# Kernel tuning notes

Measured on AMD Instinct MI355X. Metric: run time of the kernel, lower is better.

## Reference

```python
import jax, jax.numpy as jnp
import numpy as np

NBINS = 128


def setup_inputs() -> dict:
    key = jax.random.key(0)
    feats = jax.random.normal(key, (100000, 8), dtype=jnp.float32)
    return {"feats": feats}


def reference(feats):
    # feats: [N, V]. setup=True path: fmin/fmax computed from feats itself.
    nvars = feats.shape[1]
    fmin = feats.min(axis=0)  # [V]
    fmax = feats.max(axis=0)  # [V]
    # torch.linspace(min, max, nbins) per variable -> [V, NBINS]
    t = jnp.arange(NBINS, dtype=feats.dtype) / (NBINS - 1)
    lin = fmin[:, None] + (fmax - fmin)[:, None] * t[None, :]
    step = lin[:, 1] - lin[:, 0]  # [V]
    # dense diff matrix, rounded to 6 decimals (np.around = round-half-even)
    diff = jnp.round((lin[None, :, :] - feats[:, :, None]) * 1e6) / 1e6  # [N, V, NBINS]
    # torch: cur_diff[cur_diff > 0] = cur_diff.min()  (min over that var's whole [N, NBINS] slab)
    mn = diff.min(axis=(0, 2), keepdims=True)  # [1, V, 1]
    masked = jnp.where(diff > 0, mn, diff)
    bins = jnp.argmax(masked, axis=2)  # [N, V], first max like torch
    # value of the chosen bin edge per sample/var
    vals = lin[jnp.arange(nvars)[None, :], bins]  # [N, V]
    regs = jnp.clip(feats - vals, 0.0, None) / step[None, :]
    return bins, regs
```

## Files before the change

### kernel.cpp

```cpp
#include <hip/hip_runtime.h>
#include <math.h>

#define NV 8
#define NBINS 128
#define GRID_A 64
#define GRID_Q 1024
#define BLK_Q 256


__global__ __launch_bounds__(256) void k_colminmax(const float* __restrict__ feats,
                                                   float* __restrict__ ws, int n) {
    const int tid = threadIdx.x;
    const int gt = blockIdx.x * blockDim.x + tid;
    const int nth = blockDim.x * gridDim.x;
    float lmin[NV], lmax[NV];
#pragma unroll
    for (int c = 0; c < NV; ++c) { lmin[c] = __builtin_inff(); lmax[c] = -__builtin_inff(); }
    const int n4 = n >> 2;
    const float4* f4 = (const float4*)feats;
    if (((gt << 2) & 7) == 0) {
        for (int q = gt; q < n4; q += nth) {
            float4 v = f4[q];
            lmin[0] = fminf(lmin[0], v.x); lmax[0] = fmaxf(lmax[0], v.x);
            lmin[1] = fminf(lmin[1], v.y); lmax[1] = fmaxf(lmax[1], v.y);
            lmin[2] = fminf(lmin[2], v.z); lmax[2] = fmaxf(lmax[2], v.z);
            lmin[3] = fminf(lmin[3], v.w); lmax[3] = fmaxf(lmax[3], v.w);
        }
    } else {
        for (int q = gt; q < n4; q += nth) {
            float4 v = f4[q];
            lmin[4] = fminf(lmin[4], v.x); lmax[4] = fmaxf(lmax[4], v.x);
            lmin[5] = fminf(lmin[5], v.y); lmax[5] = fmaxf(lmax[5], v.y);
            lmin[6] = fminf(lmin[6], v.z); lmax[6] = fmaxf(lmax[6], v.z);
            lmin[7] = fminf(lmin[7], v.w); lmax[7] = fmaxf(lmax[7], v.w);
        }
    }
    for (int i = (n4 << 2) + gt; i < n; i += nth) {
        float v = feats[i];
        int c = i & 7;
#pragma unroll
        for (int cc = 0; cc < NV; ++cc)
            if (cc == c) { lmin[cc] = fminf(lmin[cc], v); lmax[cc] = fmaxf(lmax[cc], v); }
    }
#pragma unroll
    for (int c = 0; c < NV; ++c) {
        float mn = lmin[c], mx = lmax[c];
#pragma unroll
        for (int m = 32; m >= 1; m >>= 1) {
            mn = fminf(mn, __shfl_xor(mn, m));
            mx = fmaxf(mx, __shfl_xor(mx, m));
        }
        lmin[c] = mn; lmax[c] = mx;
    }
    __shared__ float smin[4][NV], smax[4][NV];
    const int wave = tid >> 6, lane = tid & 63;
    if (lane == 0) {
#pragma unroll
        for (int c = 0; c < NV; ++c) { smin[wave][c] = lmin[c]; smax[wave][c] = lmax[c]; }
    }
    __syncthreads();
    if (tid < NV) {
        float mn = fminf(fminf(smin[0][tid], smin[1][tid]), fminf(smin[2][tid], smin[3][tid]));
        float mx = fmaxf(fmaxf(smax[0][tid], smax[1][tid]), fmaxf(smax[2][tid], smax[3][tid]));
        ws[blockIdx.x * NV + tid] = mn;
        ws[GRID_A * NV + blockIdx.x * NV + tid] = mx;
    }
}

__global__ __launch_bounds__(BLK_Q) void k_quantize2(const float* __restrict__ feats,
                                                     const float* __restrict__ ws,
                                                     float* __restrict__ out, int n) {
    __shared__ float sgmin[NV], sgmax[NV];
    __shared__ float slin[NV * 129];
    __shared__ float sfmin[NV], sstep[NV], srstep[NV];
    const int tid = threadIdx.x;

    if (tid < 64) {
        const float4* w4 = (const float4*)ws;
        float4 a  = w4[2 * tid];
        float4 b4 = w4[2 * tid + 1];
        float4 c4 = w4[2 * GRID_A + 2 * tid];
        float4 d4 = w4[2 * GRID_A + 2 * tid + 1];
        float mn[NV] = {a.x, a.y, a.z, a.w, b4.x, b4.y, b4.z, b4.w};
        float mx[NV] = {c4.x, c4.y, c4.z, c4.w, d4.x, d4.y, d4.z, d4.w};
#pragma unroll
        for (int c = 0; c < NV; ++c) {
#pragma unroll
            for (int m = 32; m >= 1; m >>= 1) {
                mn[c] = fminf(mn[c], __shfl_xor(mn[c], m));
                mx[c] = fmaxf(mx[c], __shfl_xor(mx[c], m));
            }
        }
        if (tid == 0) {
#pragma unroll
            for (int c = 0; c < NV; ++c) { sgmin[c] = mn[c]; sgmax[c] = mx[c]; }
        }
    }
    __syncthreads();

    for (int e = tid; e < NV * NBINS; e += BLK_Q) {
        int v = e >> 7;
        int b = e & 127;
        float fmn = sgmin[v];
        float range = __fsub_rn(sgmax[v], fmn);
        float tb = __fdiv_rn((float)b, 127.0f);
        slin[v * 129 + b] = __fadd_rn(fmn, __fmul_rn(range, tb));
    }
    __syncthreads();
    if (tid < NV) {
        float s0 = slin[tid * 129 + 0];
        float s1 = slin[tid * 129 + 1];
        sfmin[tid] = s0;
        float st = __fsub_rn(s1, s0);
        sstep[tid] = st;
        srstep[tid] = __fdiv_rn(1.0f, st);
    }
    __syncthreads();

    const int gid = blockIdx.x * BLK_Q + tid;
    const int nth = GRID_Q * BLK_Q;
    const int v = gid & 7;
    const float fmn = sfmin[v];
    const float step = sstep[v];
    const float rstep = srstep[v];
    const float* lv = &slin[v * 129];
    for (int i = gid; i < n; i += nth) {
        const float feat = feats[i];
        int b = (int)floorf(__fmul_rn(__fsub_rn(feat, fmn), rstep));
        b = b < 0 ? 0 : (b > 127 ? 127 : b);
        while (b < NBINS - 1 &&
               rintf(__fmul_rn(__fsub_rn(lv[b + 1], feat), 1.0e6f)) <= 0.0f) ++b;
        while (b > 0 &&
               rintf(__fmul_rn(__fsub_rn(lv[b], feat), 1.0e6f)) > 0.0f) --b;
        const float val = lv[b];
        const float reg = __fdiv_rn(fmaxf(__fsub_rn(feat, val), 0.0f), step);
        out[i] = (float)b;
        out[n + i] = reg;
    }
}

extern "C" void kernel_launch(void* const* d_in, const int* in_sizes, int n_in,
                              void* d_out, int out_size, void* d_ws, size_t ws_size,
                              hipStream_t stream) {
    const float* feats = (const float*)d_in[0];
    float* ws = (float*)d_ws;
    float* out = (float*)d_out;
    const int n = in_sizes[0];
    k_colminmax<<<GRID_A, 256, 0, stream>>>(feats, ws, n);
    k_quantize2<<<GRID_Q, BLK_Q, 0, stream>>>(feats, ws, out, n);
}
```

Before: 67.18 us.

## Vectorize quantize with float4, prefetch inputs before setup, unroll min/max loads

The quantize kernel now handles four features per thread as float4 loads and stores. It issues the first two float4 loads before the shared-memory setup so their latency overlaps the per-block linspace construction. The grid shrinks so that two prefetched chunks cover the input. The column min/max kernel unrolls its strided loop by four to keep more loads in flight. The cost is more register pressure, plus a loop-invariant per-variable lookup that now becomes a per-element shared-memory index.

```diff
diff --git a/kernel.cpp b/kernel.cpp
--- a/kernel.cpp
+++ b/kernel.cpp
@@ -4,7 +4,7 @@
 #define NV 8
 #define NBINS 128
 #define GRID_A 64
-#define GRID_Q 1024
+#define GRID_Q 400
 #define BLK_Q 256
 
 
@@ -18,8 +18,23 @@
     for (int c = 0; c < NV; ++c) { lmin[c] = __builtin_inff(); lmax[c] = -__builtin_inff(); }
     const int n4 = n >> 2;
     const float4* f4 = (const float4*)feats;
+    int q = gt;
     if (((gt << 2) & 7) == 0) {
-        for (int q = gt; q < n4; q += nth) {
+        for (; q + 3 * nth < n4; q += 4 * nth) {
+            float4 a = f4[q];
+            float4 b = f4[q + nth];
+            float4 c = f4[q + 2 * nth];
+            float4 d = f4[q + 3 * nth];
+            lmin[0] = fminf(fminf(lmin[0], fminf(a.x, b.x)), fminf(c.x, d.x));
+            lmax[0] = fmaxf(fmaxf(lmax[0], fmaxf(a.x, b.x)), fmaxf(c.x, d.x));
+            lmin[1] = fminf(fminf(lmin[1], fminf(a.y, b.y)), fminf(c.y, d.y));
+            lmax[1] = fmaxf(fmaxf(lmax[1], fmaxf(a.y, b.y)), fmaxf(c.y, d.y));
+            lmin[2] = fminf(fminf(lmin[2], fminf(a.z, b.z)), fminf(c.z, d.z));
+            lmax[2] = fmaxf(fmaxf(lmax[2], fmaxf(a.z, b.z)), fmaxf(c.z, d.z));
+            lmin[3] = fminf(fminf(lmin[3], fminf(a.w, b.w)), fminf(c.w, d.w));
+            lmax[3] = fmaxf(fmaxf(lmax[3], fmaxf(a.w, b.w)), fmaxf(c.w, d.w));
+        }
+        for (; q < n4; q += nth) {
             float4 v = f4[q];
             lmin[0] = fminf(lmin[0], v.x); lmax[0] = fmaxf(lmax[0], v.x);
             lmin[1] = fminf(lmin[1], v.y); lmax[1] = fmaxf(lmax[1], v.y);
@@ -27,7 +42,21 @@
             lmin[3] = fminf(lmin[3], v.w); lmax[3] = fmaxf(lmax[3], v.w);
         }
     } else {
-        for (int q = gt; q < n4; q += nth) {
+        for (; q + 3 * nth < n4; q += 4 * nth) {
+            float4 a = f4[q];
+            float4 b = f4[q + nth];
+            float4 c = f4[q + 2 * nth];
+            float4 d = f4[q + 3 * nth];
+            lmin[4] = fminf(fminf(lmin[4], fminf(a.x, b.x)), fminf(c.x, d.x));
+            lmax[4] = fmaxf(fmaxf(lmax[4], fmaxf(a.x, b.x)), fmaxf(c.x, d.x));
+            lmin[5] = fminf(fminf(lmin[5], fminf(a.y, b.y)), fminf(c.y, d.y));
+            lmax[5] = fmaxf(fmaxf(lmax[5], fmaxf(a.y, b.y)), fmaxf(c.y, d.y));
+            lmin[6] = fminf(fminf(lmin[6], fminf(a.z, b.z)), fminf(c.z, d.z));
+            lmax[6] = fmaxf(fmaxf(lmax[6], fmaxf(a.z, b.z)), fmaxf(c.z, d.z));
+            lmin[7] = fminf(fminf(lmin[7], fminf(a.w, b.w)), fminf(c.w, d.w));
+            lmax[7] = fmaxf(fmaxf(lmax[7], fmaxf(a.w, b.w)), fmaxf(c.w, d.w));
+        }
+        for (; q < n4; q += nth) {
             float4 v = f4[q];
             lmin[4] = fminf(lmin[4], v.x); lmax[4] = fmaxf(lmax[4], v.x);
             lmin[5] = fminf(lmin[5], v.y); lmax[5] = fmaxf(lmax[5], v.y);
@@ -64,6 +93,42 @@
         float mx = fmaxf(fmaxf(smax[0][tid], smax[1][tid]), fmaxf(smax[2][tid], smax[3][tid]));
         ws[blockIdx.x * NV + tid] = mn;
         ws[GRID_A * NV + blockIdx.x * NV + tid] = mx;
+    }
+}
+
+__device__ __forceinline__ void proc4(float4 fv, int q, const float* __restrict__ slin,
+                                      const float* __restrict__ sfmin,
+                                      const float* __restrict__ sstep,
+                                      const float* __restrict__ srstep,
+                                      float* __restrict__ out, int n) {
+    const int v0 = (q << 2) & 7;
+    const int i0 = q << 2;
+    float fe[4] = {fv.x, fv.y, fv.z, fv.w};
+    float bins[4], regs[4];
+#pragma unroll
+    for (int j = 0; j < 4; ++j) {
+        const int v = v0 + j;
+        const float* lv = &slin[v * 129];
+        const float feat = fe[j];
+        const float fmn = sfmin[v];
+        const float step = sstep[v];
+        const float rstep = srstep[v];
+        int b = (int)floorf(__fmul_rn(__fsub_rn(feat, fmn), rstep));
+        b = b < 0 ? 0 : (b > 127 ? 127 : b);
+        while (b < NBINS - 1 &&
+               rintf(__fmul_rn(__fsub_rn(lv[b + 1], feat), 1.0e6f)) <= 0.0f) ++b;
+        while (b > 0 &&
+               rintf(__fmul_rn(__fsub_rn(lv[b], feat), 1.0e6f)) > 0.0f) --b;
+        const float val = lv[b];
+        bins[j] = (float)b;
+        regs[j] = __fdiv_rn(fmaxf(__fsub_rn(feat, val), 0.0f), step);
+    }
+    *(float4*)(out + i0) = make_float4(bins[0], bins[1], bins[2], bins[3]);
+    if ((n & 3) == 0) {
+        *(float4*)(out + n + i0) = make_float4(regs[0], regs[1], regs[2], regs[3]);
+    } else {
+        out[n + i0 + 0] = regs[0]; out[n + i0 + 1] = regs[1];
+        out[n + i0 + 2] = regs[2]; out[n + i0 + 3] = regs[3];
     }
 }
 
@@ -74,6 +139,16 @@
     __shared__ float slin[NV * 129];
     __shared__ float sfmin[NV], sstep[NV], srstep[NV];
     const int tid = threadIdx.x;
+    const int gid = blockIdx.x * BLK_Q + tid;
+    const int nth = GRID_Q * BLK_Q;
+    const int n4 = n >> 2;
+    const float4* f4 = (const float4*)feats;
+
+    const int q0 = gid, q1 = gid + nth;
+    float4 fv0, fv1;
+    const bool h0 = q0 < n4, h1 = q1 < n4;
+    if (h0) fv0 = f4[q0];
+    if (h1) fv1 = f4[q1];
 
     if (tid < 64) {
         const float4* w4 = (const float4*)ws;
@@ -117,25 +192,25 @@
     }
     __syncthreads();
 
-    const int gid = blockIdx.x * BLK_Q + tid;
-    const int nth = GRID_Q * BLK_Q;
-    const int v = gid & 7;
-    const float fmn = sfmin[v];
-    const float step = sstep[v];
-    const float rstep = srstep[v];
-    const float* lv = &slin[v * 129];
-    for (int i = gid; i < n; i += nth) {
+    if (h0) proc4(fv0, q0, slin, sfmin, sstep, srstep, out, n);
+    if (h1) proc4(fv1, q1, slin, sfmin, sstep, srstep, out, n);
+    for (int q = gid + 2 * nth; q < n4; q += nth)
+        proc4(f4[q], q, slin, sfmin, sstep, srstep, out, n);
+
+    for (int i = (n4 << 2) + gid; i < n; i += nth) {
+        const int v = i & 7;
         const float feat = feats[i];
-        int b = (int)floorf(__fmul_rn(__fsub_rn(feat, fmn), rstep));
+        const float* lv = &slin[v * 129];
+        const float fmn = sfmin[v];
+        const float step = sstep[v];
+        int b = (int)floorf(__fmul_rn(__fsub_rn(feat, fmn), srstep[v]));
         b = b < 0 ? 0 : (b > 127 ? 127 : b);
         while (b < NBINS - 1 &&
                rintf(__fmul_rn(__fsub_rn(lv[b + 1], feat), 1.0e6f)) <= 0.0f) ++b;
         while (b > 0 &&
                rintf(__fmul_rn(__fsub_rn(lv[b], feat), 1.0e6f)) > 0.0f) --b;
-        const float val = lv[b];
-        const float reg = __fdiv_rn(fmaxf(__fsub_rn(feat, val), 0.0f), step);
         out[i] = (float)b;
-        out[n + i] = reg;
+        out[n + i] = __fdiv_rn(fmaxf(__fsub_rn(feat, lv[b]), 0.0f), step);
     }
 }
 
```

Measured after the change: 65.37 us. 1.03x faster.
